# Kernel optimization log

Measured on AMD Instinct MI355X. Metric: run time of the kernel, lower is better.

Reference implementation:

```python
import jax, jax.numpy as jnp
import numpy as np

B, G, A, C = 128, 16, 8732, 21
THR = 0.5        # overlap_threshold
NEG_POS = 3      # neg_pos_ratio
VAR0, VAR1 = 0.1, 0.2  # loc_variance


def center_to_point(b):
    cxcy, wh = b[:, :2], b[:, 2:]
    return jnp.concatenate([cxcy - wh / 2, cxcy + wh / 2], axis=-1)


def iou_matrix(a, b):
    # a: [G,4], b: [A,4] point coords (x1,y1,x2,y2) -> [G,A]
    tl = jnp.maximum(a[:, None, :2], b[None, :, :2])
    br = jnp.minimum(a[:, None, 2:], b[None, :, 2:])
    wh = jnp.clip(br - tl, 0.0)
    inter = wh[..., 0] * wh[..., 1]
    area_a = (a[:, 2] - a[:, 0]) * (a[:, 3] - a[:, 1])
    area_b = (b[:, 2] - b[:, 0]) * (b[:, 3] - b[:, 1])
    return inter / (area_a[:, None] + area_b[None, :] - inter)


def encode(anchors, gt_pt):
    # anchors [A,4] (cx,cy,w,h); gt_pt [A,4] point coords
    g_cxcy = (gt_pt[:, :2] + gt_pt[:, 2:]) / 2
    g_wh = gt_pt[:, 2:] - gt_pt[:, :2]
    d_cxcy = (g_cxcy - anchors[:, :2]) / (anchors[:, 2:] * VAR0)
    d_wh = jnp.log(g_wh / anchors[:, 2:]) / VAR1
    return jnp.concatenate([d_cxcy, d_wh], axis=-1)


def match(boxes, labels, anchors, anchors_pt):
    # boxes [G,4] point coords, labels [G] int
    iou = iou_matrix(boxes, anchors_pt)           # [G,A]
    anchor_index = jnp.argmax(iou, axis=1)        # best anchor per gt, [G]
    gt_overlap = jnp.max(iou, axis=0)             # best gt overlap per anchor, [A]
    gt_index = jnp.argmax(iou, axis=0)            # best gt per anchor, [A]
    gt_overlap = gt_overlap.at[anchor_index].set(1.0)
    for i in range(G):
        gt_index = gt_index.at[anchor_index[i]].set(i)
    gt_coords = boxes[gt_index]                   # [A,4]
    loc = encode(anchors, gt_coords)              # [A,4]
    conf = labels[gt_index] + 1                   # [A], 0 reserved for background
    conf = jnp.where(gt_overlap < THR, 0, conf)
    return loc, conf


def setup_inputs() -> dict:
    key = jax.random.key(0)
    k1, k2, k3, k4, k5, k6, k7 = jax.random.split(key, 7)
    predict_offset_coords = jax.random.normal(k1, (B, A, 4), jnp.float32)
    predict_confidences = jax.random.normal(k2, (B, A, C), jnp.float32)
    # valid gt boxes: centers in [0.2,0.8], sizes in [0.05,0.3]
    c = jax.random.uniform(k3, (B, G, 2)) * 0.6 + 0.2
    s = jax.random.uniform(k4, (B, G, 2)) * 0.25 + 0.05
    target_boxes = jnp.concatenate([c - s / 2, c + s / 2], axis=-1)
    target_labels = jax.random.randint(k5, (B, G), 0, C - 1).astype(jnp.int32)
    # anchors in center-coord form (cx,cy,w,h), strictly positive w,h
    acx = jax.random.uniform(k6, (A, 2)) * 0.9 + 0.05
    awh = jax.random.uniform(k7, (A, 2)) * 0.25 + 0.05
    anchors = jnp.concatenate([acx, awh], axis=-1)
    return {"predict_offset_coords": predict_offset_coords,
            "predict_confidences": predict_confidences,
            "target_boxes": target_boxes,
            "target_labels": target_labels,
            "anchors": anchors}


def reference(predict_offset_coords, predict_confidences, target_boxes, target_labels, anchors):
    anchors_pt = center_to_point(anchors)
    loc_t, conf_t = jax.vmap(match, in_axes=(0, 0, None, None))(
        target_boxes, target_labels, anchors, anchors_pt)
    # labels are built without grad in the original (fresh tensors)
    loc_t = jax.lax.stop_gradient(loc_t)
    conf_t = jax.lax.stop_gradient(conf_t)

    is_pos = conf_t > 0                            # [B,A]
    # smooth L1 (beta=1), summed over positive anchors
    diff = predict_offset_coords - loc_t
    ad = jnp.abs(diff)
    sl1 = jnp.where(ad < 1.0, 0.5 * diff * diff, ad - 0.5)
    loss_loc = jnp.sum(sl1 * is_pos[..., None])

    num_pos = jnp.sum(is_pos, axis=1, keepdims=True)      # [B,1]
    n_total = jnp.sum(num_pos).astype(jnp.float32)
    num_neg = jnp.minimum(NEG_POS * num_pos, A - 1)        # [B,1]

    logp = jax.nn.log_softmax(predict_confidences, axis=-1)
    nll = -jnp.take_along_axis(logp, conf_t[..., None], axis=-1)[..., 0]  # [B,A]

    # hard-negative mining via double argsort
    aux = jnp.where(is_pos, 0.0, nll)
    order = jnp.argsort(-aux, axis=1)
    rank = jnp.argsort(order, axis=1)
    is_neg = rank < num_neg

    sel = jnp.logical_or(is_pos, is_neg)
    loss_cls = jnp.sum(jnp.where(sel, nll, 0.0))
    return loss_loc / n_total, loss_cls / n_total
```

## Files before the change

### kernel.cpp

```cpp
#include <hip/hip_runtime.h>
#include <math.h>

#define B_ 128
#define G_ 16
#define A_ 8732
#define C_ 21
#define THR_ 0.5f
#define NEG_POS_ 3
#define VAR0_ 0.1f
#define VAR1_ 0.2f

#define BA_    (B_ * A_)
#define NBLKL_ (BA_ / 256)

struct Accum { float loss_loc; float loss_cls; int n_total; int pad; };

__global__ void k_init(Accum* acc) {
    acc->loss_loc = 0.f;
    acc->loss_cls = 0.f;
    acc->n_total  = 0;
}

__global__ __launch_bounds__(512) void k_match(
    const float* __restrict__ tboxes,
    const int*   __restrict__ tlabels,
    const float* __restrict__ anchors,
    int*         __restrict__ match,
    int*         __restrict__ num_pos,
    Accum*                    acc)
{
    const int b    = blockIdx.x;
    const int tid  = threadIdx.x;
    const int lane = tid & 63;
    const int w    = tid >> 6;

    __shared__ float         s_ov[A_];
    __shared__ unsigned char s_gi[A_];
    __shared__ float s_boxlds[G_ * 4];
    __shared__ int   s_lab[G_];
    __shared__ unsigned long long s_gb[8 * G_];
    __shared__ int   s_forced[G_];
    __shared__ int   s_cnt[8];

    if (tid < G_ * 4) s_boxlds[tid] = tboxes[b * G_ * 4 + tid];
    if (tid < G_)     s_lab[tid]    = tlabels[b * G_ + tid];
    __syncthreads();

    float bx0[G_], by0[G_], bx1[G_], by1[G_], bar[G_];
    #pragma unroll
    for (int g = 0; g < G_; ++g) {
        bx0[g] = s_boxlds[g * 4 + 0];
        by0[g] = s_boxlds[g * 4 + 1];
        bx1[g] = s_boxlds[g * 4 + 2];
        by1[g] = s_boxlds[g * 4 + 3];
        bar[g] = (bx1[g] - bx0[g]) * (by1[g] - by0[g]);
    }

    unsigned long long gb[G_];
    #pragma unroll
    for (int g = 0; g < G_; ++g) gb[g] = 0ull;

    for (int a = tid; a < A_; a += 512) {
        float4 an = ((const float4*)anchors)[a];
        float ax0 = an.x - an.z * 0.5f, ay0 = an.y - an.w * 0.5f;
        float ax1 = an.x + an.z * 0.5f, ay1 = an.y + an.w * 0.5f;
        float area_b = (ax1 - ax0) * (ay1 - ay0);
        float bov = -1.f; int bg = 0;
        #pragma unroll
        for (int g = 0; g < G_; ++g) {
            float tlx = fmaxf(bx0[g], ax0);
            float tly = fmaxf(by0[g], ay0);
            float brx = fminf(bx1[g], ax1);
            float bry = fminf(by1[g], ay1);
            float wdt = fmaxf(brx - tlx, 0.f);
            float hgt = fmaxf(bry - tly, 0.f);
            float inter = wdt * hgt;
            float iou = inter / (bar[g] + area_b - inter);
            if (iou > bov) { bov = iou; bg = g; }
            unsigned long long pk =
                ((unsigned long long)__float_as_uint(iou) << 32) |
                (unsigned)(~(unsigned)a);
            if (pk > gb[g]) gb[g] = pk;
        }
        s_ov[a] = bov;
        s_gi[a] = (unsigned char)bg;
    }

    #pragma unroll
    for (int g = 0; g < G_; ++g) {
        #pragma unroll
        for (int off = 32; off > 0; off >>= 1) {
            unsigned long long o = __shfl_down(gb[g], off);
            if (o > gb[g]) gb[g] = o;
        }
    }
    if (lane == 0) {
        #pragma unroll
        for (int g = 0; g < G_; ++g) s_gb[w * G_ + g] = gb[g];
    }
    __syncthreads();
    if (tid < G_) {
        unsigned long long m = 0ull;
        #pragma unroll
        for (int wv = 0; wv < 8; ++wv) {
            unsigned long long v = s_gb[wv * G_ + tid];
            if (v > m) m = v;
        }
        s_forced[tid] = (int)(~(unsigned)(m & 0xFFFFFFFFull));
    }
    __syncthreads();
    if (tid == 0) {
        for (int g = 0; g < G_; ++g) {
            int a = s_forced[g];
            s_ov[a] = 1.0f;
            s_gi[a] = (unsigned char)g;
        }
    }
    __syncthreads();

    int cnt = 0;
    for (int a = tid; a < A_; a += 512) {
        float ov = s_ov[a];
        int g = s_gi[a];
        int conf = (ov < THR_) ? 0 : (s_lab[g] + 1);
        match[b * A_ + a] = conf | (g << 8);
        cnt += (conf > 0);
    }
    #pragma unroll
    for (int off = 32; off > 0; off >>= 1) cnt += __shfl_down(cnt, off);
    if (lane == 0) s_cnt[w] = cnt;
    __syncthreads();
    if (tid == 0) {
        int t = 0;
        #pragma unroll
        for (int wv = 0; wv < 8; ++wv) t += s_cnt[wv];
        num_pos[b] = t;
        atomicAdd(&acc->n_total, t);
    }
}

__global__ __launch_bounds__(256) void k_loss(
    const float* __restrict__ pred_off,
    const float* __restrict__ pred_conf,
    const float* __restrict__ tboxes,
    const float* __restrict__ anchors,
    const int*   __restrict__ match,
    float*       __restrict__ aux,
    float*       __restrict__ part_loc,
    float*       __restrict__ part_cls)
{
    const int tid  = threadIdx.x;
    const int i    = blockIdx.x * 256 + tid;
    const int lane = tid & 63;
    const int w    = tid >> 6;

    __shared__ float4 s_conf4[(256 * C_) / 4];
    __shared__ float  s_lloc[4];
    __shared__ float  s_pnll[4];

    const float4* g4 = (const float4*)pred_conf + (size_t)blockIdx.x * (256 * C_ / 4);
    #pragma unroll
    for (int k = 0; k < 6; ++k) {
        int idx = tid + k * 256;
        if (idx < 256 * C_ / 4) s_conf4[idx] = g4[idx];
    }
    __syncthreads();

    const float* sc = (const float*)s_conf4 + tid * C_;

    int mk   = match[i];
    int conf = mk & 0xff;
    int g    = mk >> 8;

    float m = sc[0];
    #pragma unroll
    for (int c = 1; c < C_; ++c) m = fmaxf(m, sc[c]);
    float s = 0.f;
    #pragma unroll
    for (int c = 0; c < C_; ++c) s += __expf(sc[c] - m);
    float lse = m + __logf(s);

    float xc  = sc[conf];
    float nll = lse - xc;
    bool  pos = conf > 0;

    float lloc = 0.f, pnll = 0.f;
    aux[i] = pos ? 0.f : nll;

    if (pos) {
        pnll = nll;
        int b = i / A_;
        int a = i - b * A_;
        float4 an = ((const float4*)anchors)[a];
        float4 bx = ((const float4*)tboxes)[b * G_ + g];
        float gcx = (bx.x + bx.z) * 0.5f, gcy = (bx.y + bx.w) * 0.5f;
        float gw = bx.z - bx.x, gh = bx.w - bx.y;
        float l0 = (gcx - an.x) / (an.z * VAR0_);
        float l1 = (gcy - an.y) / (an.w * VAR0_);
        float l2 = logf(gw / an.z) / VAR1_;
        float l3 = logf(gh / an.w) / VAR1_;
        float4 p = ((const float4*)pred_off)[i];
        float d, ad;
        d = p.x - l0; ad = fabsf(d); lloc += (ad < 1.f) ? 0.5f * d * d : ad - 0.5f;
        d = p.y - l1; ad = fabsf(d); lloc += (ad < 1.f) ? 0.5f * d * d : ad - 0.5f;
        d = p.z - l2; ad = fabsf(d); lloc += (ad < 1.f) ? 0.5f * d * d : ad - 0.5f;
        d = p.w - l3; ad = fabsf(d); lloc += (ad < 1.f) ? 0.5f * d * d : ad - 0.5f;
    }

    #pragma unroll
    for (int off = 32; off > 0; off >>= 1) {
        lloc += __shfl_down(lloc, off);
        pnll += __shfl_down(pnll, off);
    }
    if (lane == 0) { s_lloc[w] = lloc; s_pnll[w] = pnll; }
    __syncthreads();
    if (tid == 0) {
        part_loc[blockIdx.x] = s_lloc[0] + s_lloc[1] + s_lloc[2] + s_lloc[3];
        part_cls[blockIdx.x] = s_pnll[0] + s_pnll[1] + s_pnll[2] + s_pnll[3];
    }
}

#define NPT_ 35
__global__ __launch_bounds__(256) void k_select(
    const float* __restrict__ aux,
    const int*   __restrict__ num_pos,
    Accum*                    acc)
{
    const int b    = blockIdx.x;
    const int tid  = threadIdx.x;
    const int lane = tid & 63;
    const int w    = tid >> 6;

    __shared__ int   s_c[2][4];
    __shared__ int   s_cf[4];
    __shared__ float s_sf[4];

    unsigned u[NPT_];
    #pragma unroll
    for (int j = 0; j < NPT_; ++j) {
        int a = tid + j * 256;
        u[j] = (a < A_) ? __float_as_uint(aux[(size_t)b * A_ + a]) : 0u;
    }

    const int K = min(NEG_POS_ * num_pos[b], A_ - 1);

    unsigned lo = 0u, hi = 0x7f800000u;
    int it = 0;
    while (lo < hi) {
        unsigned mid = (lo + hi) >> 1;
        int c = 0;
        #pragma unroll
        for (int j = 0; j < NPT_; ++j) c += (u[j] > mid);
        #pragma unroll
        for (int off = 32; off > 0; off >>= 1) c += __shfl_down(c, off);
        if (lane == 0) s_c[it & 1][w] = c;
        __syncthreads();
        int total = s_c[it & 1][0] + s_c[it & 1][1] + s_c[it & 1][2] + s_c[it & 1][3];
        if (total >= K) lo = mid + 1; else hi = mid;
        ++it;
    }

    int c = 0; float sm = 0.f;
    #pragma unroll
    for (int j = 0; j < NPT_; ++j) {
        if (u[j] > lo) { c++; sm += __uint_as_float(u[j]); }
    }
    #pragma unroll
    for (int off = 32; off > 0; off >>= 1) {
        c  += __shfl_down(c, off);
        sm += __shfl_down(sm, off);
    }
    if (lane == 0) { s_cf[w] = c; s_sf[w] = sm; }
    __syncthreads();
    if (tid == 0) {
        int   ct = s_cf[0] + s_cf[1] + s_cf[2] + s_cf[3];
        float st = s_sf[0] + s_sf[1] + s_sf[2] + s_sf[3];
        float T = __uint_as_float(lo);
        atomicAdd(&acc->loss_cls, st + (float)(K - ct) * T);
    }
}

__global__ __launch_bounds__(256) void k_final(
    const Accum* __restrict__ acc,
    const float* __restrict__ part_loc,
    const float* __restrict__ part_cls,
    float*       __restrict__ out)
{
    const int tid  = threadIdx.x;
    const int lane = tid & 63;
    const int w    = tid >> 6;
    __shared__ float s_l[4], s_cl[4];

    float L = 0.f, Cc = 0.f;
    for (int i = tid; i < NBLKL_; i += 256) { L += part_loc[i]; Cc += part_cls[i]; }
    #pragma unroll
    for (int off = 32; off > 0; off >>= 1) {
        L  += __shfl_down(L, off);
        Cc += __shfl_down(Cc, off);
    }
    if (lane == 0) { s_l[w] = L; s_cl[w] = Cc; }
    __syncthreads();
    if (tid == 0) {
        float n = (float)acc->n_total;
        float lloc = s_l[0] + s_l[1] + s_l[2] + s_l[3];
        float lcls = s_cl[0] + s_cl[1] + s_cl[2] + s_cl[3] + acc->loss_cls;
        out[0] = lloc / n;
        out[1] = lcls / n;
    }
}

extern "C" void kernel_launch(void* const* d_in, const int* in_sizes, int n_in,
                              void* d_out, int out_size, void* d_ws, size_t ws_size,
                              hipStream_t stream) {
    const float* pred_off  = (const float*)d_in[0];
    const float* pred_conf = (const float*)d_in[1];
    const float* tboxes    = (const float*)d_in[2];
    const int*   tlabels   = (const int*)  d_in[3];
    const float* anchors   = (const float*)d_in[4];
    float* out = (float*)d_out;

    char* ws = (char*)d_ws;
    int*   match_ws = (int*)ws;     ws += (size_t)BA_ * sizeof(int);
    float* aux_ws   = (float*)ws;   ws += (size_t)BA_ * sizeof(float);
    float* ploc_ws  = (float*)ws;   ws += (size_t)((NBLKL_ + 3) & ~3) * sizeof(float);
    float* pcls_ws  = (float*)ws;   ws += (size_t)((NBLKL_ + 3) & ~3) * sizeof(float);
    int*   npos_ws  = (int*)ws;     ws += (size_t)((B_ + 3) & ~3) * sizeof(int);
    Accum* acc      = (Accum*)ws;

    k_init<<<1, 1, 0, stream>>>(acc);
    k_match<<<B_, 512, 0, stream>>>(tboxes, tlabels, anchors, match_ws, npos_ws, acc);
    k_loss<<<NBLKL_, 256, 0, stream>>>(pred_off, pred_conf, tboxes, anchors,
                                       match_ws, aux_ws, ploc_ws, pcls_ws);
    k_select<<<B_, 256, 0, stream>>>(aux_ws, npos_ws, acc);
    k_final<<<1, 256, 0, stream>>>(acc, ploc_ws, pcls_ws, out);
}
```

Baseline: 227.3 us.

## Fuse matching, softmax loss and hard-negative selection into one per-image kernel

Merges the match, loss and select kernels into a single kernel with one 512-thread block per image. Each block streams that image's confidences through shared memory in 512-anchor chunks and keeps the per-anchor overlap, gt index and negative loss in LDS for the radix-style threshold search. This removes the global match and aux round trips, the atomics and several launches. In exchange the grid shrinks from thousands of blocks to 128, fewer than the number of CUs. The heavy confidence read then runs with low parallelism, each chunk load is followed by a barrier, and the large LDS footprint limits occupancy to about one block per CU.

Measured after the change: 265.8 us. 1.17x slower.

```diff
diff --git a/kernel.cpp b/kernel.cpp
--- a/kernel.cpp
+++ b/kernel.cpp
@@ -10,24 +10,22 @@
 #define VAR0_ 0.1f
 #define VAR1_ 0.2f
 
-#define BA_    (B_ * A_)
-#define NBLKL_ (BA_ / 256)
-
-struct Accum { float loss_loc; float loss_cls; int n_total; int pad; };
-
-__global__ void k_init(Accum* acc) {
-    acc->loss_loc = 0.f;
-    acc->loss_cls = 0.f;
-    acc->n_total  = 0;
-}
-
-__global__ __launch_bounds__(512) void k_match(
+#define CHUNK_  512
+#define NCHUNK_ ((A_ + CHUNK_ - 1) / CHUNK_)
+#define TAILA_  (A_ - (NCHUNK_ - 1) * CHUNK_)
+#define FULLV_  (CHUNK_ * C_ / 4)
+#define TAILV_  (TAILA_ * C_ / 4)
+#define NPT_    NCHUNK_
+
+__global__ __launch_bounds__(512) void k_fused(
+    const float* __restrict__ pred_off,
+    const float* __restrict__ pred_conf,
     const float* __restrict__ tboxes,
     const int*   __restrict__ tlabels,
     const float* __restrict__ anchors,
-    int*         __restrict__ match,
-    int*         __restrict__ num_pos,
-    Accum*                    acc)
+    float*       __restrict__ lloc_b,
+    float*       __restrict__ lcls_b,
+    int*         __restrict__ npos_b)
 {
     const int b    = blockIdx.x;
     const int tid  = threadIdx.x;
@@ -36,11 +34,16 @@
 
     __shared__ float         s_ov[A_];
     __shared__ unsigned char s_gi[A_];
+    __shared__ float         s_aux[A_];
+    __shared__ float4        s_stage[FULLV_];
     __shared__ float s_boxlds[G_ * 4];
     __shared__ int   s_lab[G_];
     __shared__ unsigned long long s_gb[8 * G_];
     __shared__ int   s_forced[G_];
     __shared__ int   s_cnt[8];
+    __shared__ int   s_c[2][8];
+    __shared__ float s_r0[8], s_r1[8], s_r3[8];
+    __shared__ int   s_r2[8];
 
     if (tid < G_ * 4) s_boxlds[tid] = tboxes[b * G_ * 4 + tid];
     if (tid < G_)     s_lab[tid]    = tlabels[b * G_ + tid];
@@ -116,133 +119,80 @@
             s_gi[a] = (unsigned char)g;
         }
     }
-    __syncthreads();
-
-    int cnt = 0;
-    for (int a = tid; a < A_; a += 512) {
-        float ov = s_ov[a];
-        int g = s_gi[a];
-        int conf = (ov < THR_) ? 0 : (s_lab[g] + 1);
-        match[b * A_ + a] = conf | (g << 8);
-        cnt += (conf > 0);
-    }
-    #pragma unroll
-    for (int off = 32; off > 0; off >>= 1) cnt += __shfl_down(cnt, off);
-    if (lane == 0) s_cnt[w] = cnt;
-    __syncthreads();
-    if (tid == 0) {
-        int t = 0;
-        #pragma unroll
-        for (int wv = 0; wv < 8; ++wv) t += s_cnt[wv];
-        num_pos[b] = t;
-        atomicAdd(&acc->n_total, t);
-    }
-}
-
-__global__ __launch_bounds__(256) void k_loss(
-    const float* __restrict__ pred_off,
-    const float* __restrict__ pred_conf,
-    const float* __restrict__ tboxes,
-    const float* __restrict__ anchors,
-    const int*   __restrict__ match,
-    float*       __restrict__ aux,
-    float*       __restrict__ part_loc,
-    float*       __restrict__ part_cls)
-{
-    const int tid  = threadIdx.x;
-    const int i    = blockIdx.x * 256 + tid;
-    const int lane = tid & 63;
-    const int w    = tid >> 6;
-
-    __shared__ float4 s_conf4[(256 * C_) / 4];
-    __shared__ float  s_lloc[4];
-    __shared__ float  s_pnll[4];
-
-    const float4* g4 = (const float4*)pred_conf + (size_t)blockIdx.x * (256 * C_ / 4);
-    #pragma unroll
-    for (int k = 0; k < 6; ++k) {
-        int idx = tid + k * 256;
-        if (idx < 256 * C_ / 4) s_conf4[idx] = g4[idx];
-    }
-    __syncthreads();
-
-    const float* sc = (const float*)s_conf4 + tid * C_;
-
-    int mk   = match[i];
-    int conf = mk & 0xff;
-    int g    = mk >> 8;
-
-    float m = sc[0];
-    #pragma unroll
-    for (int c = 1; c < C_; ++c) m = fmaxf(m, sc[c]);
-    float s = 0.f;
-    #pragma unroll
-    for (int c = 0; c < C_; ++c) s += __expf(sc[c] - m);
-    float lse = m + __logf(s);
-
-    float xc  = sc[conf];
-    float nll = lse - xc;
-    bool  pos = conf > 0;
 
     float lloc = 0.f, pnll = 0.f;
-    aux[i] = pos ? 0.f : nll;
-
-    if (pos) {
-        pnll = nll;
-        int b = i / A_;
-        int a = i - b * A_;
-        float4 an = ((const float4*)anchors)[a];
-        float4 bx = ((const float4*)tboxes)[b * G_ + g];
-        float gcx = (bx.x + bx.z) * 0.5f, gcy = (bx.y + bx.w) * 0.5f;
-        float gw = bx.z - bx.x, gh = bx.w - bx.y;
-        float l0 = (gcx - an.x) / (an.z * VAR0_);
-        float l1 = (gcy - an.y) / (an.w * VAR0_);
-        float l2 = logf(gw / an.z) / VAR1_;
-        float l3 = logf(gh / an.w) / VAR1_;
-        float4 p = ((const float4*)pred_off)[i];
-        float d, ad;
-        d = p.x - l0; ad = fabsf(d); lloc += (ad < 1.f) ? 0.5f * d * d : ad - 0.5f;
-        d = p.y - l1; ad = fabsf(d); lloc += (ad < 1.f) ? 0.5f * d * d : ad - 0.5f;
-        d = p.z - l2; ad = fabsf(d); lloc += (ad < 1.f) ? 0.5f * d * d : ad - 0.5f;
-        d = p.w - l3; ad = fabsf(d); lloc += (ad < 1.f) ? 0.5f * d * d : ad - 0.5f;
-    }
-
-    #pragma unroll
-    for (int off = 32; off > 0; off >>= 1) {
-        lloc += __shfl_down(lloc, off);
-        pnll += __shfl_down(pnll, off);
-    }
-    if (lane == 0) { s_lloc[w] = lloc; s_pnll[w] = pnll; }
-    __syncthreads();
-    if (tid == 0) {
-        part_loc[blockIdx.x] = s_lloc[0] + s_lloc[1] + s_lloc[2] + s_lloc[3];
-        part_cls[blockIdx.x] = s_pnll[0] + s_pnll[1] + s_pnll[2] + s_pnll[3];
-    }
-}
-
-#define NPT_ 35
-__global__ __launch_bounds__(256) void k_select(
-    const float* __restrict__ aux,
-    const int*   __restrict__ num_pos,
-    Accum*                    acc)
-{
-    const int b    = blockIdx.x;
-    const int tid  = threadIdx.x;
-    const int lane = tid & 63;
-    const int w    = tid >> 6;
-
-    __shared__ int   s_c[2][4];
-    __shared__ int   s_cf[4];
-    __shared__ float s_sf[4];
+    int   cnt  = 0;
+
+    for (int cc = 0; cc < NCHUNK_; ++cc) {
+        const int nv = (cc == NCHUNK_ - 1) ? TAILV_ : FULLV_;
+        __syncthreads();
+        const float4* g4 = (const float4*)pred_conf
+                         + ((((size_t)b * A_) + (size_t)cc * CHUNK_) * C_ >> 2);
+        for (int idx = tid; idx < nv; idx += 512) s_stage[idx] = g4[idx];
+        __syncthreads();
+
+        const int a = cc * CHUNK_ + tid;
+        float auxv = 0.f;
+        if (a < A_) {
+            const float* sc = (const float*)s_stage + tid * C_;
+            float m = sc[0];
+            #pragma unroll
+            for (int c = 1; c < C_; ++c) m = fmaxf(m, sc[c]);
+            float s = 0.f;
+            #pragma unroll
+            for (int c = 0; c < C_; ++c) s += __expf(sc[c] - m);
+            float lse = m + __logf(s);
+
+            float ov  = s_ov[a];
+            int   g   = s_gi[a];
+            int  conf = (ov < THR_) ? 0 : (s_lab[g] + 1);
+            float xc  = sc[conf];
+            float nll = lse - xc;
+            bool  pos = conf > 0;
+            auxv = pos ? 0.f : nll;
+
+            if (pos) {
+                cnt++;
+                pnll += nll;
+                float4 an = ((const float4*)anchors)[a];
+                float bxx0 = s_boxlds[g * 4 + 0], bxy0 = s_boxlds[g * 4 + 1];
+                float bxx1 = s_boxlds[g * 4 + 2], bxy1 = s_boxlds[g * 4 + 3];
+                float gcx = (bxx0 + bxx1) * 0.5f, gcy = (bxy0 + bxy1) * 0.5f;
+                float gw = bxx1 - bxx0, gh = bxy1 - bxy0;
+                float l0 = (gcx - an.x) / (an.z * VAR0_);
+                float l1 = (gcy - an.y) / (an.w * VAR0_);
+                float l2 = logf(gw / an.z) / VAR1_;
+                float l3 = logf(gh / an.w) / VAR1_;
+                float4 p = ((const float4*)pred_off)[(size_t)b * A_ + a];
+                float d, ad;
+                d = p.x - l0; ad = fabsf(d); lloc += (ad < 1.f) ? 0.5f * d * d : ad - 0.5f;
+                d = p.y - l1; ad = fabsf(d); lloc += (ad < 1.f) ? 0.5f * d * d : ad - 0.5f;
+                d = p.z - l2; ad = fabsf(d); lloc += (ad < 1.f) ? 0.5f * d * d : ad - 0.5f;
+                d = p.w - l3; ad = fabsf(d); lloc += (ad < 1.f) ? 0.5f * d * d : ad - 0.5f;
+            }
+        }
+        if (a < A_) s_aux[a] = auxv;
+    }
+
+    {
+        int c = cnt;
+        #pragma unroll
+        for (int off = 32; off > 0; off >>= 1) c += __shfl_down(c, off);
+        if (lane == 0) s_cnt[w] = c;
+    }
+    __syncthreads();
+    int npos = 0;
+    #pragma unroll
+    for (int wv = 0; wv < 8; ++wv) npos += s_cnt[wv];
+    if (tid == 0) npos_b[b] = npos;
+    const int K = min(NEG_POS_ * npos, A_ - 1);
 
     unsigned u[NPT_];
     #pragma unroll
     for (int j = 0; j < NPT_; ++j) {
-        int a = tid + j * 256;
-        u[j] = (a < A_) ? __float_as_uint(aux[(size_t)b * A_ + a]) : 0u;
-    }
-
-    const int K = min(NEG_POS_ * num_pos[b], A_ - 1);
+        int a = tid + j * 512;
+        u[j] = (a < A_) ? __float_as_uint(s_aux[a]) : 0u;
+    }
 
     unsigned lo = 0u, hi = 0x7f800000u;
     int it = 0;
@@ -255,57 +205,67 @@
         for (int off = 32; off > 0; off >>= 1) c += __shfl_down(c, off);
         if (lane == 0) s_c[it & 1][w] = c;
         __syncthreads();
-        int total = s_c[it & 1][0] + s_c[it & 1][1] + s_c[it & 1][2] + s_c[it & 1][3];
+        int total = 0;
+        #pragma unroll
+        for (int wv = 0; wv < 8; ++wv) total += s_c[it & 1][wv];
         if (total >= K) lo = mid + 1; else hi = mid;
         ++it;
     }
 
-    int c = 0; float sm = 0.f;
+    int selc = 0; float selsm = 0.f;
     #pragma unroll
     for (int j = 0; j < NPT_; ++j) {
-        if (u[j] > lo) { c++; sm += __uint_as_float(u[j]); }
-    }
+        if (u[j] > lo) { selc++; selsm += __uint_as_float(u[j]); }
+    }
+
     #pragma unroll
     for (int off = 32; off > 0; off >>= 1) {
-        c  += __shfl_down(c, off);
-        sm += __shfl_down(sm, off);
-    }
-    if (lane == 0) { s_cf[w] = c; s_sf[w] = sm; }
+        lloc  += __shfl_down(lloc, off);
+        pnll  += __shfl_down(pnll, off);
+        selc  += __shfl_down(selc, off);
+        selsm += __shfl_down(selsm, off);
+    }
+    if (lane == 0) { s_r0[w] = lloc; s_r1[w] = pnll; s_r2[w] = selc; s_r3[w] = selsm; }
     __syncthreads();
     if (tid == 0) {
-        int   ct = s_cf[0] + s_cf[1] + s_cf[2] + s_cf[3];
-        float st = s_sf[0] + s_sf[1] + s_sf[2] + s_sf[3];
+        float L = 0.f, P = 0.f, S = 0.f; int Cc = 0;
+        #pragma unroll
+        for (int wv = 0; wv < 8; ++wv) {
+            L += s_r0[wv]; P += s_r1[wv]; Cc += s_r2[wv]; S += s_r3[wv];
+        }
         float T = __uint_as_float(lo);
-        atomicAdd(&acc->loss_cls, st + (float)(K - ct) * T);
+        lloc_b[b] = L;
+        lcls_b[b] = P + S + (float)(K - Cc) * T;
     }
 }
 
-__global__ __launch_bounds__(256) void k_final(
-    const Accum* __restrict__ acc,
-    const float* __restrict__ part_loc,
-    const float* __restrict__ part_cls,
+__global__ __launch_bounds__(128) void k_fin(
+    const float* __restrict__ lloc_b,
+    const float* __restrict__ lcls_b,
+    const int*   __restrict__ npos_b,
     float*       __restrict__ out)
 {
     const int tid  = threadIdx.x;
     const int lane = tid & 63;
     const int w    = tid >> 6;
-    __shared__ float s_l[4], s_cl[4];
-
-    float L = 0.f, Cc = 0.f;
-    for (int i = tid; i < NBLKL_; i += 256) { L += part_loc[i]; Cc += part_cls[i]; }
+    __shared__ float s_l[2], s_c[2];
+    __shared__ int   s_n[2];
+
+    float L = lloc_b[tid];
+    float Cc = lcls_b[tid];
+    int   n = npos_b[tid];
     #pragma unroll
     for (int off = 32; off > 0; off >>= 1) {
         L  += __shfl_down(L, off);
         Cc += __shfl_down(Cc, off);
-    }
-    if (lane == 0) { s_l[w] = L; s_cl[w] = Cc; }
+        n  += __shfl_down(n, off);
+    }
+    if (lane == 0) { s_l[w] = L; s_c[w] = Cc; s_n[w] = n; }
     __syncthreads();
     if (tid == 0) {
-        float n = (float)acc->n_total;
-        float lloc = s_l[0] + s_l[1] + s_l[2] + s_l[3];
-        float lcls = s_cl[0] + s_cl[1] + s_cl[2] + s_cl[3] + acc->loss_cls;
-        out[0] = lloc / n;
-        out[1] = lcls / n;
+        float ntot = (float)(s_n[0] + s_n[1]);
+        out[0] = (s_l[0] + s_l[1]) / ntot;
+        out[1] = (s_c[0] + s_c[1]) / ntot;
     }
 }
 
@@ -320,17 +280,11 @@
     float* out = (float*)d_out;
 
     char* ws = (char*)d_ws;
-    int*   match_ws = (int*)ws;     ws += (size_t)BA_ * sizeof(int);
-    float* aux_ws   = (float*)ws;   ws += (size_t)BA_ * sizeof(float);
-    float* ploc_ws  = (float*)ws;   ws += (size_t)((NBLKL_ + 3) & ~3) * sizeof(float);
-    float* pcls_ws  = (float*)ws;   ws += (size_t)((NBLKL_ + 3) & ~3) * sizeof(float);
-    int*   npos_ws  = (int*)ws;     ws += (size_t)((B_ + 3) & ~3) * sizeof(int);
-    Accum* acc      = (Accum*)ws;
-
-    k_init<<<1, 1, 0, stream>>>(acc);
-    k_match<<<B_, 512, 0, stream>>>(tboxes, tlabels, anchors, match_ws, npos_ws, acc);
-    k_loss<<<NBLKL_, 256, 0, stream>>>(pred_off, pred_conf, tboxes, anchors,
-                                       match_ws, aux_ws, ploc_ws, pcls_ws);
-    k_select<<<B_, 256, 0, stream>>>(aux_ws, npos_ws, acc);
-    k_final<<<1, 256, 0, stream>>>(acc, ploc_ws, pcls_ws, out);
+    float* lloc_ws = (float*)ws;  ws += (size_t)B_ * sizeof(float);
+    float* lcls_ws = (float*)ws;  ws += (size_t)B_ * sizeof(float);
+    int*   npos_ws = (int*)ws;
+
+    k_fused<<<B_, 512, 0, stream>>>(pred_off, pred_conf, tboxes, tlabels, anchors,
+                                    lloc_ws, lcls_ws, npos_ws);
+    k_fin<<<1, 128, 0, stream>>>(lloc_ws, lcls_ws, npos_ws, out);
 }
```

## Fuse match, loss, select and final reduction into one cooperative kernel

Applied to the files above, without the earlier changes.

Replaces the five separate launches (init, match, loss, select, final) with a single cooperative kernel of 256 blocks of 512 threads, separated by grid-wide syncs. The loss phase becomes a persistent grid-stride loop over 512-anchor chunks, with register prefetch and a double-buffered LDS stage for the confidence logits. Per-block partials replace atomics and are reduced in the final phase. This removes launch overhead and atomics but adds grid syncs, leaves only 256 blocks for the bandwidth-heavy loss phase, and raises the LDS footprint to roughly 130 KB per block, which limits occupancy.

Measured after the change: 334.3 us. 1.47x slower.

```diff
diff --git a/kernel.cpp b/kernel.cpp
--- a/kernel.cpp
+++ b/kernel.cpp
@@ -1,5 +1,8 @@
 #include <hip/hip_runtime.h>
+#include <hip/hip_cooperative_groups.h>
 #include <math.h>
+
+namespace cg = cooperative_groups;
 
 #define B_ 128
 #define G_ 16
@@ -11,301 +14,313 @@
 #define VAR1_ 0.2f
 
 #define BA_    (B_ * A_)
-#define NBLKL_ (BA_ / 256)
-
-struct Accum { float loss_loc; float loss_cls; int n_total; int pad; };
-
-__global__ void k_init(Accum* acc) {
-    acc->loss_loc = 0.f;
-    acc->loss_cls = 0.f;
-    acc->n_total  = 0;
-}
-
-__global__ __launch_bounds__(512) void k_match(
+#define GRID_  256
+#define CHA_   512
+#define NCH_   (BA_ / CHA_)
+#define CV4_   (CHA_ * C_ / 4)
+#define NPT_   ((A_ + 511) / 512)
+
+__global__ __launch_bounds__(512) void k_all(
+    const float* __restrict__ pred_off,
+    const float* __restrict__ pred_conf,
     const float* __restrict__ tboxes,
     const int*   __restrict__ tlabels,
     const float* __restrict__ anchors,
     int*         __restrict__ match,
-    int*         __restrict__ num_pos,
-    Accum*                    acc)
+    float*       __restrict__ aux,
+    int*         __restrict__ npos_b,
+    float*       __restrict__ ploc_b,
+    float*       __restrict__ pcls_b,
+    float*       __restrict__ scls_b,
+    float*       __restrict__ out)
 {
-    const int b    = blockIdx.x;
+    cg::grid_group gridg = cg::this_grid();
     const int tid  = threadIdx.x;
     const int lane = tid & 63;
     const int w    = tid >> 6;
+    const int bid  = blockIdx.x;
 
     __shared__ float         s_ov[A_];
     __shared__ unsigned char s_gi[A_];
+    __shared__ float4        s_stage[2][CV4_];
     __shared__ float s_boxlds[G_ * 4];
     __shared__ int   s_lab[G_];
     __shared__ unsigned long long s_gb[8 * G_];
     __shared__ int   s_forced[G_];
     __shared__ int   s_cnt[8];
-
-    if (tid < G_ * 4) s_boxlds[tid] = tboxes[b * G_ * 4 + tid];
-    if (tid < G_)     s_lab[tid]    = tlabels[b * G_ + tid];
-    __syncthreads();
-
-    float bx0[G_], by0[G_], bx1[G_], by1[G_], bar[G_];
-    #pragma unroll
-    for (int g = 0; g < G_; ++g) {
-        bx0[g] = s_boxlds[g * 4 + 0];
-        by0[g] = s_boxlds[g * 4 + 1];
-        bx1[g] = s_boxlds[g * 4 + 2];
-        by1[g] = s_boxlds[g * 4 + 3];
-        bar[g] = (bx1[g] - bx0[g]) * (by1[g] - by0[g]);
+    __shared__ int   s_c[2][8];
+    __shared__ float s_r0[8], s_r1[8], s_r3[8];
+    __shared__ int   s_r2[8];
+
+    if (bid < B_) {
+        const int b = bid;
+        if (tid < G_ * 4) s_boxlds[tid] = tboxes[b * G_ * 4 + tid];
+        if (tid < G_)     s_lab[tid]    = tlabels[b * G_ + tid];
+        __syncthreads();
+
+        float bx0[G_], by0[G_], bx1[G_], by1[G_], bar[G_];
+        #pragma unroll
+        for (int g = 0; g < G_; ++g) {
+            bx0[g] = s_boxlds[g * 4 + 0];
+            by0[g] = s_boxlds[g * 4 + 1];
+            bx1[g] = s_boxlds[g * 4 + 2];
+            by1[g] = s_boxlds[g * 4 + 3];
+            bar[g] = (bx1[g] - bx0[g]) * (by1[g] - by0[g]);
+        }
+
+        unsigned long long gb[G_];
+        #pragma unroll
+        for (int g = 0; g < G_; ++g) gb[g] = 0ull;
+
+        for (int a = tid; a < A_; a += 512) {
+            float4 an = ((const float4*)anchors)[a];
+            float ax0 = an.x - an.z * 0.5f, ay0 = an.y - an.w * 0.5f;
+            float ax1 = an.x + an.z * 0.5f, ay1 = an.y + an.w * 0.5f;
+            float area_b = (ax1 - ax0) * (ay1 - ay0);
+            float bov = -1.f; int bg = 0;
+            #pragma unroll
+            for (int g = 0; g < G_; ++g) {
+                float tlx = fmaxf(bx0[g], ax0);
+                float tly = fmaxf(by0[g], ay0);
+                float brx = fminf(bx1[g], ax1);
+                float bry = fminf(by1[g], ay1);
+                float wdt = fmaxf(brx - tlx, 0.f);
+                float hgt = fmaxf(bry - tly, 0.f);
+                float inter = wdt * hgt;
+                float iou = inter / (bar[g] + area_b - inter);
+                if (iou > bov) { bov = iou; bg = g; }
+                unsigned long long pk =
+                    ((unsigned long long)__float_as_uint(iou) << 32) |
+                    (unsigned)(~(unsigned)a);
+                if (pk > gb[g]) gb[g] = pk;
+            }
+            s_ov[a] = bov;
+            s_gi[a] = (unsigned char)bg;
+        }
+
+        #pragma unroll
+        for (int g = 0; g < G_; ++g) {
+            #pragma unroll
+            for (int off = 32; off > 0; off >>= 1) {
+                unsigned long long o = __shfl_down(gb[g], off);
+                if (o > gb[g]) gb[g] = o;
+            }
+        }
+        if (lane == 0) {
+            #pragma unroll
+            for (int g = 0; g < G_; ++g) s_gb[w * G_ + g] = gb[g];
+        }
+        __syncthreads();
+        if (tid < G_) {
+            unsigned long long m = 0ull;
+            #pragma unroll
+            for (int wv = 0; wv < 8; ++wv) {
+                unsigned long long v = s_gb[wv * G_ + tid];
+                if (v > m) m = v;
+            }
+            s_forced[tid] = (int)(~(unsigned)(m & 0xFFFFFFFFull));
+        }
+        __syncthreads();
+        if (tid == 0) {
+            for (int g = 0; g < G_; ++g) {
+                int a = s_forced[g];
+                s_ov[a] = 1.0f;
+                s_gi[a] = (unsigned char)g;
+            }
+        }
+        __syncthreads();
+
+        int cnt = 0;
+        for (int a = tid; a < A_; a += 512) {
+            float ov = s_ov[a];
+            int g = s_gi[a];
+            int conf = (ov < THR_) ? 0 : (s_lab[g] + 1);
+            match[b * A_ + a] = conf | (g << 8);
+            cnt += (conf > 0);
+        }
+        #pragma unroll
+        for (int off = 32; off > 0; off >>= 1) cnt += __shfl_down(cnt, off);
+        if (lane == 0) s_cnt[w] = cnt;
+        __syncthreads();
+        if (tid == 0) {
+            int t = 0;
+            #pragma unroll
+            for (int wv = 0; wv < 8; ++wv) t += s_cnt[wv];
+            npos_b[b] = t;
+        }
     }
-
-    unsigned long long gb[G_];
-    #pragma unroll
-    for (int g = 0; g < G_; ++g) gb[g] = 0ull;
-
-    for (int a = tid; a < A_; a += 512) {
-        float4 an = ((const float4*)anchors)[a];
-        float ax0 = an.x - an.z * 0.5f, ay0 = an.y - an.w * 0.5f;
-        float ax1 = an.x + an.z * 0.5f, ay1 = an.y + an.w * 0.5f;
-        float area_b = (ax1 - ax0) * (ay1 - ay0);
-        float bov = -1.f; int bg = 0;
-        #pragma unroll
-        for (int g = 0; g < G_; ++g) {
-            float tlx = fmaxf(bx0[g], ax0);
-            float tly = fmaxf(by0[g], ay0);
-            float brx = fminf(bx1[g], ax1);
-            float bry = fminf(by1[g], ay1);
-            float wdt = fmaxf(brx - tlx, 0.f);
-            float hgt = fmaxf(bry - tly, 0.f);
-            float inter = wdt * hgt;
-            float iou = inter / (bar[g] + area_b - inter);
-            if (iou > bov) { bov = iou; bg = g; }
-            unsigned long long pk =
-                ((unsigned long long)__float_as_uint(iou) << 32) |
-                (unsigned)(~(unsigned)a);
-            if (pk > gb[g]) gb[g] = pk;
-        }
-        s_ov[a] = bov;
-        s_gi[a] = (unsigned char)bg;
+    gridg.sync();
+
+    {
+        float lloc = 0.f, pnll = 0.f;
+        const float4* gbase = (const float4*)pred_conf;
+        float4 r[6];
+        int c = bid;
+
+        #pragma unroll
+        for (int j = 0; j < 6; ++j) {
+            int idx = tid + j * 512;
+            if (idx < CV4_) r[j] = gbase[(size_t)c * CV4_ + idx];
+        }
+        int mkcur = match[c * CHA_ + tid];
+        #pragma unroll
+        for (int j = 0; j < 6; ++j) {
+            int idx = tid + j * 512;
+            if (idx < CV4_) s_stage[0][idx] = r[j];
+        }
+        __syncthreads();
+
+        int k = 0;
+        for (; c < NCH_; c += GRID_, ++k) {
+            const int cn = c + GRID_;
+            const bool hasnext = cn < NCH_;
+            int mknext = 0;
+            if (hasnext) {
+                #pragma unroll
+                for (int j = 0; j < 6; ++j) {
+                    int idx = tid + j * 512;
+                    if (idx < CV4_) r[j] = gbase[(size_t)cn * CV4_ + idx];
+                }
+                mknext = match[cn * CHA_ + tid];
+            }
+
+            const float* sc = (const float*)&s_stage[k & 1][0] + tid * C_;
+            float m = sc[0];
+            #pragma unroll
+            for (int cc = 1; cc < C_; ++cc) m = fmaxf(m, sc[cc]);
+            float s = 0.f;
+            #pragma unroll
+            for (int cc = 0; cc < C_; ++cc) s += __expf(sc[cc] - m);
+            float lse = m + __logf(s);
+
+            const int i    = c * CHA_ + tid;
+            const int conf = mkcur & 0xff;
+            const int g    = mkcur >> 8;
+            float xc  = sc[conf];
+            float nll = lse - xc;
+            bool  pos = conf > 0;
+            aux[i] = pos ? 0.f : nll;
+
+            if (pos) {
+                pnll += nll;
+                int b = i / A_;
+                int a = i - b * A_;
+                float4 an = ((const float4*)anchors)[a];
+                float4 bx = ((const float4*)tboxes)[b * G_ + g];
+                float gcx = (bx.x + bx.z) * 0.5f, gcy = (bx.y + bx.w) * 0.5f;
+                float gw = bx.z - bx.x, gh = bx.w - bx.y;
+                float l0 = (gcx - an.x) / (an.z * VAR0_);
+                float l1 = (gcy - an.y) / (an.w * VAR0_);
+                float l2 = logf(gw / an.z) / VAR1_;
+                float l3 = logf(gh / an.w) / VAR1_;
+                float4 p = ((const float4*)pred_off)[i];
+                float d, ad;
+                d = p.x - l0; ad = fabsf(d); lloc += (ad < 1.f) ? 0.5f * d * d : ad - 0.5f;
+                d = p.y - l1; ad = fabsf(d); lloc += (ad < 1.f) ? 0.5f * d * d : ad - 0.5f;
+                d = p.z - l2; ad = fabsf(d); lloc += (ad < 1.f) ? 0.5f * d * d : ad - 0.5f;
+                d = p.w - l3; ad = fabsf(d); lloc += (ad < 1.f) ? 0.5f * d * d : ad - 0.5f;
+            }
+
+            __syncthreads();
+            if (hasnext) {
+                #pragma unroll
+                for (int j = 0; j < 6; ++j) {
+                    int idx = tid + j * 512;
+                    if (idx < CV4_) s_stage[(k + 1) & 1][idx] = r[j];
+                }
+                mkcur = mknext;
+                __syncthreads();
+            }
+        }
+
+        #pragma unroll
+        for (int off = 32; off > 0; off >>= 1) {
+            lloc += __shfl_down(lloc, off);
+            pnll += __shfl_down(pnll, off);
+        }
+        if (lane == 0) { s_r0[w] = lloc; s_r1[w] = pnll; }
+        __syncthreads();
+        if (tid == 0) {
+            float L = 0.f, P = 0.f;
+            #pragma unroll
+            for (int wv = 0; wv < 8; ++wv) { L += s_r0[wv]; P += s_r1[wv]; }
+            ploc_b[bid] = L;
+            pcls_b[bid] = P;
+        }
     }
-
-    #pragma unroll
-    for (int g = 0; g < G_; ++g) {
+    gridg.sync();
+
+    if (bid < B_) {
+        const int b = bid;
+        unsigned u[NPT_];
+        #pragma unroll
+        for (int j = 0; j < NPT_; ++j) {
+            int a = tid + j * 512;
+            u[j] = (a < A_) ? __float_as_uint(aux[(size_t)b * A_ + a]) : 0u;
+        }
+
+        const int K = min(NEG_POS_ * npos_b[b], A_ - 1);
+
+        unsigned lo = 0u, hi = 0x7f800000u;
+        int it = 0;
+        while (lo < hi) {
+            unsigned mid = (lo + hi) >> 1;
+            int cx = 0;
+            #pragma unroll
+            for (int j = 0; j < NPT_; ++j) cx += (u[j] > mid);
+            #pragma unroll
+            for (int off = 32; off > 0; off >>= 1) cx += __shfl_down(cx, off);
+            if (lane == 0) s_c[it & 1][w] = cx;
+            __syncthreads();
+            int total = 0;
+            #pragma unroll
+            for (int wv = 0; wv < 8; ++wv) total += s_c[it & 1][wv];
+            if (total >= K) lo = mid + 1; else hi = mid;
+            ++it;
+        }
+
+        int selc = 0; float selsm = 0.f;
+        #pragma unroll
+        for (int j = 0; j < NPT_; ++j) {
+            if (u[j] > lo) { selc++; selsm += __uint_as_float(u[j]); }
+        }
         #pragma unroll
         for (int off = 32; off > 0; off >>= 1) {
-            unsigned long long o = __shfl_down(gb[g], off);
-            if (o > gb[g]) gb[g] = o;
+            selc  += __shfl_down(selc, off);
+            selsm += __shfl_down(selsm, off);
+        }
+        if (lane == 0) { s_r2[w] = selc; s_r3[w] = selsm; }
+        __syncthreads();
+        if (tid == 0) {
+            int ct = 0; float st = 0.f;
+            #pragma unroll
+            for (int wv = 0; wv < 8; ++wv) { ct += s_r2[wv]; st += s_r3[wv]; }
+            float T = __uint_as_float(lo);
+            scls_b[b] = st + (float)(K - ct) * T;
         }
     }
-    if (lane == 0) {
-        #pragma unroll
-        for (int g = 0; g < G_; ++g) s_gb[w * G_ + g] = gb[g];
-    }
-    __syncthreads();
-    if (tid < G_) {
-        unsigned long long m = 0ull;
-        #pragma unroll
-        for (int wv = 0; wv < 8; ++wv) {
-            unsigned long long v = s_gb[wv * G_ + tid];
-            if (v > m) m = v;
-        }
-        s_forced[tid] = (int)(~(unsigned)(m & 0xFFFFFFFFull));
-    }
-    __syncthreads();
-    if (tid == 0) {
-        for (int g = 0; g < G_; ++g) {
-            int a = s_forced[g];
-            s_ov[a] = 1.0f;
-            s_gi[a] = (unsigned char)g;
-        }
-    }
-    __syncthreads();
-
-    int cnt = 0;
-    for (int a = tid; a < A_; a += 512) {
-        float ov = s_ov[a];
-        int g = s_gi[a];
-        int conf = (ov < THR_) ? 0 : (s_lab[g] + 1);
-        match[b * A_ + a] = conf | (g << 8);
-        cnt += (conf > 0);
-    }
-    #pragma unroll
-    for (int off = 32; off > 0; off >>= 1) cnt += __shfl_down(cnt, off);
-    if (lane == 0) s_cnt[w] = cnt;
-    __syncthreads();
-    if (tid == 0) {
-        int t = 0;
-        #pragma unroll
-        for (int wv = 0; wv < 8; ++wv) t += s_cnt[wv];
-        num_pos[b] = t;
-        atomicAdd(&acc->n_total, t);
-    }
-}
-
-__global__ __launch_bounds__(256) void k_loss(
-    const float* __restrict__ pred_off,
-    const float* __restrict__ pred_conf,
-    const float* __restrict__ tboxes,
-    const float* __restrict__ anchors,
-    const int*   __restrict__ match,
-    float*       __restrict__ aux,
-    float*       __restrict__ part_loc,
-    float*       __restrict__ part_cls)
-{
-    const int tid  = threadIdx.x;
-    const int i    = blockIdx.x * 256 + tid;
-    const int lane = tid & 63;
-    const int w    = tid >> 6;
-
-    __shared__ float4 s_conf4[(256 * C_) / 4];
-    __shared__ float  s_lloc[4];
-    __shared__ float  s_pnll[4];
-
-    const float4* g4 = (const float4*)pred_conf + (size_t)blockIdx.x * (256 * C_ / 4);
-    #pragma unroll
-    for (int k = 0; k < 6; ++k) {
-        int idx = tid + k * 256;
-        if (idx < 256 * C_ / 4) s_conf4[idx] = g4[idx];
-    }
-    __syncthreads();
-
-    const float* sc = (const float*)s_conf4 + tid * C_;
-
-    int mk   = match[i];
-    int conf = mk & 0xff;
-    int g    = mk >> 8;
-
-    float m = sc[0];
-    #pragma unroll
-    for (int c = 1; c < C_; ++c) m = fmaxf(m, sc[c]);
-    float s = 0.f;
-    #pragma unroll
-    for (int c = 0; c < C_; ++c) s += __expf(sc[c] - m);
-    float lse = m + __logf(s);
-
-    float xc  = sc[conf];
-    float nll = lse - xc;
-    bool  pos = conf > 0;
-
-    float lloc = 0.f, pnll = 0.f;
-    aux[i] = pos ? 0.f : nll;
-
-    if (pos) {
-        pnll = nll;
-        int b = i / A_;
-        int a = i - b * A_;
-        float4 an = ((const float4*)anchors)[a];
-        float4 bx = ((const float4*)tboxes)[b * G_ + g];
-        float gcx = (bx.x + bx.z) * 0.5f, gcy = (bx.y + bx.w) * 0.5f;
-        float gw = bx.z - bx.x, gh = bx.w - bx.y;
-        float l0 = (gcx - an.x) / (an.z * VAR0_);
-        float l1 = (gcy - an.y) / (an.w * VAR0_);
-        float l2 = logf(gw / an.z) / VAR1_;
-        float l3 = logf(gh / an.w) / VAR1_;
-        float4 p = ((const float4*)pred_off)[i];
-        float d, ad;
-        d = p.x - l0; ad = fabsf(d); lloc += (ad < 1.f) ? 0.5f * d * d : ad - 0.5f;
-        d = p.y - l1; ad = fabsf(d); lloc += (ad < 1.f) ? 0.5f * d * d : ad - 0.5f;
-        d = p.z - l2; ad = fabsf(d); lloc += (ad < 1.f) ? 0.5f * d * d : ad - 0.5f;
-        d = p.w - l3; ad = fabsf(d); lloc += (ad < 1.f) ? 0.5f * d * d : ad - 0.5f;
-    }
-
-    #pragma unroll
-    for (int off = 32; off > 0; off >>= 1) {
-        lloc += __shfl_down(lloc, off);
-        pnll += __shfl_down(pnll, off);
-    }
-    if (lane == 0) { s_lloc[w] = lloc; s_pnll[w] = pnll; }
-    __syncthreads();
-    if (tid == 0) {
-        part_loc[blockIdx.x] = s_lloc[0] + s_lloc[1] + s_lloc[2] + s_lloc[3];
-        part_cls[blockIdx.x] = s_pnll[0] + s_pnll[1] + s_pnll[2] + s_pnll[3];
-    }
-}
-
-#define NPT_ 35
-__global__ __launch_bounds__(256) void k_select(
-    const float* __restrict__ aux,
-    const int*   __restrict__ num_pos,
-    Accum*                    acc)
-{
-    const int b    = blockIdx.x;
-    const int tid  = threadIdx.x;
-    const int lane = tid & 63;
-    const int w    = tid >> 6;
-
-    __shared__ int   s_c[2][4];
-    __shared__ int   s_cf[4];
-    __shared__ float s_sf[4];
-
-    unsigned u[NPT_];
-    #pragma unroll
-    for (int j = 0; j < NPT_; ++j) {
-        int a = tid + j * 256;
-        u[j] = (a < A_) ? __float_as_uint(aux[(size_t)b * A_ + a]) : 0u;
-    }
-
-    const int K = min(NEG_POS_ * num_pos[b], A_ - 1);
-
-    unsigned lo = 0u, hi = 0x7f800000u;
-    int it = 0;
-    while (lo < hi) {
-        unsigned mid = (lo + hi) >> 1;
-        int c = 0;
-        #pragma unroll
-        for (int j = 0; j < NPT_; ++j) c += (u[j] > mid);
-        #pragma unroll
-        for (int off = 32; off > 0; off >>= 1) c += __shfl_down(c, off);
-        if (lane == 0) s_c[it & 1][w] = c;
-        __syncthreads();
-        int total = s_c[it & 1][0] + s_c[it & 1][1] + s_c[it & 1][2] + s_c[it & 1][3];
-        if (total >= K) lo = mid + 1; else hi = mid;
-        ++it;
-    }
-
-    int c = 0; float sm = 0.f;
-    #pragma unroll
-    for (int j = 0; j < NPT_; ++j) {
-        if (u[j] > lo) { c++; sm += __uint_as_float(u[j]); }
-    }
-    #pragma unroll
-    for (int off = 32; off > 0; off >>= 1) {
-        c  += __shfl_down(c, off);
-        sm += __shfl_down(sm, off);
-    }
-    if (lane == 0) { s_cf[w] = c; s_sf[w] = sm; }
-    __syncthreads();
-    if (tid == 0) {
-        int   ct = s_cf[0] + s_cf[1] + s_cf[2] + s_cf[3];
-        float st = s_sf[0] + s_sf[1] + s_sf[2] + s_sf[3];
-        float T = __uint_as_float(lo);
-        atomicAdd(&acc->loss_cls, st + (float)(K - ct) * T);
-    }
-}
-
-__global__ __launch_bounds__(256) void k_final(
-    const Accum* __restrict__ acc,
-    const float* __restrict__ part_loc,
-    const float* __restrict__ part_cls,
-    float*       __restrict__ out)
-{
-    const int tid  = threadIdx.x;
-    const int lane = tid & 63;
-    const int w    = tid >> 6;
-    __shared__ float s_l[4], s_cl[4];
-
-    float L = 0.f, Cc = 0.f;
-    for (int i = tid; i < NBLKL_; i += 256) { L += part_loc[i]; Cc += part_cls[i]; }
-    #pragma unroll
-    for (int off = 32; off > 0; off >>= 1) {
-        L  += __shfl_down(L, off);
-        Cc += __shfl_down(Cc, off);
-    }
-    if (lane == 0) { s_l[w] = L; s_cl[w] = Cc; }
-    __syncthreads();
-    if (tid == 0) {
-        float n = (float)acc->n_total;
-        float lloc = s_l[0] + s_l[1] + s_l[2] + s_l[3];
-        float lcls = s_cl[0] + s_cl[1] + s_cl[2] + s_cl[3] + acc->loss_cls;
-        out[0] = lloc / n;
-        out[1] = lcls / n;
+    gridg.sync();
+
+    if (bid == 0) {
+        float L  = (tid < GRID_) ? ploc_b[tid] : 0.f;
+        float Cc = (tid < GRID_) ? pcls_b[tid] : 0.f;
+        if (tid < B_) Cc += scls_b[tid];
+        float n  = (tid < B_) ? (float)npos_b[tid] : 0.f;
+        #pragma unroll
+        for (int off = 32; off > 0; off >>= 1) {
+            L  += __shfl_down(L, off);
+            Cc += __shfl_down(Cc, off);
+            n  += __shfl_down(n, off);
+        }
+        if (lane == 0) { s_r0[w] = L; s_r1[w] = Cc; s_r3[w] = n; }
+        __syncthreads();
+        if (tid == 0) {
+            float Lt = 0.f, Ct = 0.f, Nt = 0.f;
+            #pragma unroll
+            for (int wv = 0; wv < 8; ++wv) { Lt += s_r0[wv]; Ct += s_r1[wv]; Nt += s_r3[wv]; }
+            out[0] = Lt / Nt;
+            out[1] = Ct / Nt;
+        }
     }
 }
 
@@ -320,17 +335,20 @@
     float* out = (float*)d_out;
 
     char* ws = (char*)d_ws;
-    int*   match_ws = (int*)ws;     ws += (size_t)BA_ * sizeof(int);
-    float* aux_ws   = (float*)ws;   ws += (size_t)BA_ * sizeof(float);
-    float* ploc_ws  = (float*)ws;   ws += (size_t)((NBLKL_ + 3) & ~3) * sizeof(float);
-    float* pcls_ws  = (float*)ws;   ws += (size_t)((NBLKL_ + 3) & ~3) * sizeof(float);
-    int*   npos_ws  = (int*)ws;     ws += (size_t)((B_ + 3) & ~3) * sizeof(int);
-    Accum* acc      = (Accum*)ws;
-
-    k_init<<<1, 1, 0, stream>>>(acc);
-    k_match<<<B_, 512, 0, stream>>>(tboxes, tlabels, anchors, match_ws, npos_ws, acc);
-    k_loss<<<NBLKL_, 256, 0, stream>>>(pred_off, pred_conf, tboxes, anchors,
-                                       match_ws, aux_ws, ploc_ws, pcls_ws);
-    k_select<<<B_, 256, 0, stream>>>(aux_ws, npos_ws, acc);
-    k_final<<<1, 256, 0, stream>>>(acc, ploc_ws, pcls_ws, out);
+    int*   match_ws = (int*)ws;   ws += (size_t)BA_ * sizeof(int);
+    float* aux_ws   = (float*)ws; ws += (size_t)BA_ * sizeof(float);
+    float* ploc_ws  = (float*)ws; ws += (size_t)GRID_ * sizeof(float);
+    float* pcls_ws  = (float*)ws; ws += (size_t)GRID_ * sizeof(float);
+    float* scls_ws  = (float*)ws; ws += (size_t)B_ * sizeof(float);
+    int*   npos_ws  = (int*)ws;
+
+    void* args[] = {
+        (void*)&pred_off, (void*)&pred_conf, (void*)&tboxes,
+        (void*)&tlabels,  (void*)&anchors,
+        (void*)&match_ws, (void*)&aux_ws, (void*)&npos_ws,
+        (void*)&ploc_ws,  (void*)&pcls_ws, (void*)&scls_ws,
+        (void*)&out
+    };
+    hipLaunchCooperativeKernel((void*)k_all, dim3(GRID_), dim3(512),
+                               args, 0, stream);
 }
```
